# Performance work log

Measured on AMD Instinct MI355X. Metric: run time of the kernel, lower is better.

The kernel has to match this reference:

```python
import jax, jax.numpy as jnp
import numpy as np

N_NODES = 10000
N_EDGES = 160000
IN_DIM, HID_DIM, OUT_DIM = 256, 512, 256


def gcn_conv(x, W, b, src, dst, dinv):
    # PyG GCNConv with add_self_loops=True and symmetric normalization.
    # dinv = deg^{-1/2} computed once (degrees include self loops).
    h = x @ W                                   # [N, F_out]
    norm = dinv[src] * dinv[dst]                # [E]
    msg = h[src] * norm[:, None]                # gather + scale, [E, F_out]
    agg = jnp.zeros_like(h).at[dst].add(msg)    # scatter-add over edges
    agg = agg + h * (dinv * dinv)[:, None]      # self-loop contribution
    return agg + b


def setup_inputs() -> dict:
    key = jax.random.key(0)
    ks = jax.random.split(key, 8)
    x = jax.random.normal(ks[0], (N_NODES, IN_DIM), dtype=jnp.float32)
    edge_index = jax.random.randint(ks[1], (2, N_EDGES), 0, N_NODES, dtype=jnp.int64)

    def glorot(k, fan_in, fan_out):
        s = jnp.sqrt(6.0 / (fan_in + fan_out)).astype(jnp.float32)
        return jax.random.uniform(k, (fan_in, fan_out), jnp.float32, -s, s)

    return {
        "x": x,
        "W1": glorot(ks[2], IN_DIM, HID_DIM), "b1": jnp.zeros((HID_DIM,), jnp.float32),
        "W2": glorot(ks[3], HID_DIM, HID_DIM), "b2": jnp.zeros((HID_DIM,), jnp.float32),
        "W3": glorot(ks[4], HID_DIM, OUT_DIM), "b3": jnp.zeros((OUT_DIM,), jnp.float32),
        "edge_index": edge_index,
    }


def reference(x, W1, b1, W2, b2, W3, b3, edge_index):
    src, dst = edge_index[0], edge_index[1]
    n = x.shape[0]
    # degree with self loops (edge weight 1), shared by all three layers
    deg = jnp.zeros((n,), x.dtype).at[dst].add(1.0) + 1.0
    dinv = jax.lax.rsqrt(deg)
    h = jnp.tanh(gcn_conv(x, W1, b1, src, dst, dinv))
    h = jnp.tanh(gcn_conv(h, W2, b2, src, dst, dinv))
    out = gcn_conv(h, W3, b3, src, dst, dinv)
    return out
```

## Files before the change

kernel.cpp:

```cpp
#include <hip/hip_runtime.h>
#include <math.h>

#define NN 10000
#define NE 160000
#define IN_DIM 256
#define HID_DIM 512
#define OUT_DIM 256

typedef unsigned short u16;
typedef _Float16 f16x8 __attribute__((ext_vector_type(8)));
typedef __attribute__((ext_vector_type(4))) float f32x4;


union F16U { _Float16 h; u16 u; };
static __device__ __forceinline__ u16 f2h_bits(float f) {
    F16U v; v.h = (_Float16)f; return v.u;
}
static __device__ __forceinline__ float h2f(u16 b) {
    F16U v; v.u = b; return (float)v.h;
}


__global__ void k_init(const float* __restrict__ W1, const float* __restrict__ W2,
                       const float* __restrict__ W3,
                       u16* __restrict__ W1h, u16* __restrict__ W1l,
                       u16* __restrict__ W2h, u16* __restrict__ W2l,
                       u16* __restrict__ W3h, u16* __restrict__ W3l,
                       int* __restrict__ deg) {
    int idx = blockIdx.x * blockDim.x + threadIdx.x;
    const int S1 = IN_DIM * HID_DIM;
    const int S2 = HID_DIM * HID_DIM;
    const int S3 = HID_DIM * OUT_DIM;
    const int TW = S1 + S2 + S3;
    if (idx < TW) {
        const float* W; u16 *Th, *Tl; int K, N, local;
        if (idx < S1)           { W = W1; Th = W1h; Tl = W1l; K = IN_DIM;  N = HID_DIM; local = idx; }
        else if (idx < S1 + S2) { W = W2; Th = W2h; Tl = W2l; K = HID_DIM; N = HID_DIM; local = idx - S1; }
        else                    { W = W3; Th = W3h; Tl = W3l; K = HID_DIM; N = OUT_DIM; local = idx - S1 - S2; }
        int k = local / N, n = local - k * N;
        float v = W[local];
        F16U hh; hh.h = (_Float16)v;
        float r = (v - (float)hh.h) * 2048.0f;
        Th[(size_t)n * K + k] = hh.u;
        Tl[(size_t)n * K + k] = f2h_bits(r);
    } else if (idx < TW + NN) {
        deg[idx - TW] = 0;
    }
}


__global__ void k_count_deg(const int* __restrict__ dst, int* __restrict__ deg) {
    int e = blockIdx.x * blockDim.x + threadIdx.x;
    if (e < NE) atomicAdd(&deg[dst[e]], 1);
}

__launch_bounds__(1024)
__global__ void k_scan(const int* __restrict__ deg, int* __restrict__ row,
                       int* __restrict__ csr, float* __restrict__ dinv) {
    __shared__ int sdeg[10240];
    __shared__ int sums[1024];
    const int tid = threadIdx.x;
    for (int i = tid; i < NN; i += 1024) sdeg[i] = deg[i];
    __syncthreads();
    const int CH = 10;
    int base = tid * CH;
    int s = 0;
    for (int j = 0; j < CH; ++j) {
        int i = base + j;
        if (i < NN) s += sdeg[i] + 1;
    }
    sums[tid] = s;
    __syncthreads();
    for (int off = 1; off < 1024; off <<= 1) {
        int t = (tid >= off) ? sums[tid - off] : 0;
        __syncthreads();
        sums[tid] += t;
        __syncthreads();
    }
    int run = sums[tid] - s;
    for (int j = 0; j < CH; ++j) {
        int i = base + j;
        if (i < NN) {
            int dg = sdeg[i];
            csr[run] = i;
            row[i] = run + 1;
            dinv[i] = rsqrtf((float)dg + 1.0f);
            run += dg + 1;
        }
    }
}

__global__ void k_fill(const int* __restrict__ src, const int* __restrict__ dst,
                       int* __restrict__ row, int* __restrict__ csr) {
    int e = blockIdx.x * blockDim.x + threadIdx.x;
    if (e < NE) {
        int pos = atomicAdd(&row[dst[e]], 1);
        csr[pos] = src[e];
    }
}


struct PfSet { uint4 a0, a1, bh, bl; };

template<int K, bool HAS_BIAS, bool DO_TANH, bool F16_OUT, bool ROWSCALE>
__launch_bounds__(256)
__global__ void k_gemm_f16x2(const u16* __restrict__ A, const u16* __restrict__ Bhi,
                             const u16* __restrict__ Blo,
                             const float* __restrict__ bias, const float* __restrict__ rowscale,
                             float* __restrict__ C, u16* __restrict__ Ch,
                             int M, int N, int MT, int MT8) {
    __shared__ uint4 As[2][512];
    __shared__ uint4 BsH[2][256];
    __shared__ uint4 BsL[2][256];

    const int id = blockIdx.x;
    const int xcd = id & 7;
    const int q2 = id >> 3;
    const int mt = (q2 % MT8) * 8 + xcd;
    const int nt = q2 / MT8;
    if (mt >= MT) return;

    const int tid  = threadIdx.x;
    const int wave = tid >> 6;
    const int lane = tid & 63;
    const int lr   = lane & 15;
    const int quad = lane >> 4;
    const int m_base = mt * 128;
    const int n_base = nt * 64;

    const int s_row = tid >> 2;
    const int s_kq  = tid & 3;
    const int c_lo  = ((s_row >> 4) << 6) + s_kq * 16 + (s_row & 15);

    const u16* pA0 = A   + (size_t)(m_base + s_row) * K + s_kq * 8;
    const u16* pA1 = pA0 + (size_t)64 * K;
    const u16* pBh = Bhi + (size_t)(n_base + s_row) * K + s_kq * 8;
    const u16* pBl = Blo + (size_t)(n_base + s_row) * K + s_kq * 8;
    const bool g0 = (m_base + s_row) < M;
    const bool g1 = (m_base + s_row + 64) < M;

    const uint4 z = make_uint4(0u, 0u, 0u, 0u);

    auto load_set = [&](int it, PfSet& r) {
        const int ko = it * 32;
        r.a0 = z; r.a1 = z;
        if (g0) r.a0 = *(const uint4*)(pA0 + ko);
        if (g1) r.a1 = *(const uint4*)(pA1 + ko);
        r.bh = *(const uint4*)(pBh + ko);
        r.bl = *(const uint4*)(pBl + ko);
    };
    auto lds_write = [&](int buf, const PfSet& r) {
        As[buf][c_lo] = r.a0;
        As[buf][c_lo + 256] = r.a1;
        BsH[buf][c_lo] = r.bh;
        BsL[buf][c_lo] = r.bl;
    };

    f32x4 accH[2][4] = {};
    f32x4 accL[2][4] = {};

    auto compute = [&](int buf) {
        f16x8 a[2], bH[4], bL[4];
#pragma unroll
        for (int tm = 0; tm < 2; ++tm) {
            int c = (wave * 2 + tm) * 64 + lane;
            a[tm] = *(const f16x8*)&As[buf][c];
        }
#pragma unroll
        for (int tn = 0; tn < 4; ++tn) {
            int c = tn * 64 + lane;
            bH[tn] = *(const f16x8*)&BsH[buf][c];
            bL[tn] = *(const f16x8*)&BsL[buf][c];
        }
#pragma unroll
        for (int tm = 0; tm < 2; ++tm)
#pragma unroll
            for (int tn = 0; tn < 4; ++tn) {
                accH[tm][tn] = __builtin_amdgcn_mfma_f32_16x16x32_f16(a[tm], bH[tn], accH[tm][tn], 0, 0, 0);
                accL[tm][tn] = __builtin_amdgcn_mfma_f32_16x16x32_f16(a[tm], bL[tn], accL[tm][tn], 0, 0, 0);
            }
    };

    const int NIT = K >> 5;
    PfSet sA;

    load_set(0, sA);
    lds_write(0, sA);
    __syncthreads();

    for (int it = 0; it < NIT; ++it) {
        const bool has_next = (it + 1) < NIT;
        PfSet sN;
        if (has_next) load_set(it + 1, sN);
        compute(it & 1);
        if (has_next) lds_write((it + 1) & 1, sN);
        __syncthreads();
    }

#pragma unroll
    for (int tm = 0; tm < 2; ++tm) {
        int row0 = m_base + wave * 32 + tm * 16 + quad * 4;
#pragma unroll
        for (int i = 0; i < 4; ++i) {
            int row = row0 + i;
            if (row >= M) continue;
            float rs = ROWSCALE ? rowscale[row] : 1.0f;
#pragma unroll
            for (int tn = 0; tn < 4; ++tn) {
                int col = n_base + tn * 16 + lr;
                float v = accH[tm][tn][i] + accL[tm][tn][i] * (1.0f / 2048.0f);
                if (HAS_BIAS) v += bias[col];
                if (DO_TANH) v = tanhf(v);
                if (ROWSCALE) v *= rs;
                if (F16_OUT) {
                    Ch[(size_t)row * N + col] = f2h_bits(v);
                } else {
                    C[(size_t)row * N + col] = v;
                }
            }
        }
    }
}


template<bool PRESCALED, bool HAS_BIAS, bool F16_OUT, int F4>
__launch_bounds__(256)
__global__ void k_gather(const float* __restrict__ h, const float* __restrict__ dinv,
                         const int* __restrict__ row_end, const int* __restrict__ csr,
                         const float* __restrict__ bias,
                         float* __restrict__ outF, u16* __restrict__ outH) {
    constexpr int NS = 8;
    constexpr int F4S = F4 / NS;
    constexpr int NPB = 256 / F4S;
    const int slice = blockIdx.x & (NS - 1);
    const int g = blockIdx.x >> 3;
    const int tid = threadIdx.x;
    const int d = g * NPB + tid / F4S;
    if (d >= NN) return;
    const int f = slice * F4S + (tid & (F4S - 1));

    const int start = (d == 0) ? 0 : row_end[d - 1];
    const int end = row_end[d];
    const float4* h4 = (const float4*)h;

    float ax = 0.f, ay = 0.f, az = 0.f, aw = 0.f;
    int e = start;
    for (; e + 8 <= end; e += 8) {
        int s[8]; float4 v[8]; float w[8];
#pragma unroll
        for (int j = 0; j < 8; ++j) s[j] = csr[e + j];
#pragma unroll
        for (int j = 0; j < 8; ++j) v[j] = h4[(size_t)s[j] * F4 + f];
#pragma unroll
        for (int j = 0; j < 8; ++j) w[j] = PRESCALED ? 1.0f : dinv[s[j]];
#pragma unroll
        for (int j = 0; j < 8; ++j) {
            ax += w[j] * v[j].x; ay += w[j] * v[j].y;
            az += w[j] * v[j].z; aw += w[j] * v[j].w;
        }
    }
    for (; e < end; ++e) {
        int s = csr[e];
        float w = PRESCALED ? 1.0f : dinv[s];
        float4 v = h4[(size_t)s * F4 + f];
        ax += w * v.x; ay += w * v.y; az += w * v.z; aw += w * v.w;
    }

    const float dd = dinv[d];
    float rx = dd * ax, ry = dd * ay, rz = dd * az, rw = dd * aw;
    if (HAS_BIAS) {
        float4 bv = ((const float4*)bias)[f];
        rx += bv.x; ry += bv.y; rz += bv.z; rw += bv.w;
    }
    if (F16_OUT) {
        ushort4 vh = make_ushort4(f2h_bits(rx), f2h_bits(ry), f2h_bits(rz), f2h_bits(rw));
        ((ushort4*)outH)[(size_t)d * F4 + f] = vh;
    } else {
        ((float4*)outF)[(size_t)d * F4 + f] = make_float4(rx, ry, rz, rw);
    }
}


extern "C" void kernel_launch(void* const* d_in, const int* in_sizes, int n_in,
                              void* d_out, int out_size, void* d_ws, size_t ws_size,
                              hipStream_t stream) {
    const float* x  = (const float*)d_in[0];
    const float* W1 = (const float*)d_in[1];
    const float* b1 = (const float*)d_in[2];
    const float* W2 = (const float*)d_in[3];
    const float* b2 = (const float*)d_in[4];
    const float* W3 = (const float*)d_in[5];
    const float* b3 = (const float*)d_in[6];
    const int* edge = (const int*)d_in[7];
    const int* src = edge;
    const int* dst = edge + NE;
    float* out = (float*)d_out;

    const size_t SLOT = (size_t)NN * HID_DIM * 4;
    char* p = (char*)d_ws;
    char* slot0 = p;
    char* slot1 = p + SLOT;
    char* q = p + 2 * SLOT;
    u16* W1Th = (u16*)q; q += (size_t)IN_DIM  * HID_DIM * 2;
    u16* W1Tl = (u16*)q; q += (size_t)IN_DIM  * HID_DIM * 2;
    u16* W2Th = (u16*)q; q += (size_t)HID_DIM * HID_DIM * 2;
    u16* W2Tl = (u16*)q; q += (size_t)HID_DIM * HID_DIM * 2;
    u16* W3Th = (u16*)q; q += (size_t)HID_DIM * OUT_DIM * 2;
    u16* W3Tl = (u16*)q; q += (size_t)HID_DIM * OUT_DIM * 2;
    int*   deg  = (int*)q;   q += (size_t)NN * 4;
    float* dinv = (float*)q; q += (size_t)NN * 4;
    int*   row  = (int*)q;   q += (size_t)NN * 4;
    int*   csr  = (int*)q;   q += (size_t)(NE + NN) * 4;

    u16* Xagg   = (u16*)slot0;
    float* g1   = (float*)slot1;
    u16* H1agg  = (u16*)slot0;
    u16* h2     = (u16*)slot1;
    float* g3   = (float*)slot0;

    const int T = 256;
    const int MT = (NN + 127) / 128;
    const int MT8 = (MT + 7) / 8;

    {
        int total = IN_DIM * HID_DIM + HID_DIM * HID_DIM + HID_DIM * OUT_DIM + NN;
        k_init<<<(total + T - 1) / T, T, 0, stream>>>(W1, W2, W3, W1Th, W1Tl,
                                                      W2Th, W2Tl, W3Th, W3Tl, deg);
    }
    k_count_deg<<<(NE + T - 1) / T, T, 0, stream>>>(dst, deg);
    k_scan<<<1, 1024, 0, stream>>>(deg, row, csr, dinv);
    k_fill<<<(NE + T - 1) / T, T, 0, stream>>>(src, dst, row, csr);

    const int G256 = ((NN + 31) / 32) * 8;
    const int G512 = ((NN + 15) / 16) * 8;
    const int GEMM_G512 = 8 * MT8 * (HID_DIM / 64);
    const int GEMM_G256 = 8 * MT8 * (OUT_DIM / 64);

    k_gather<false, false, true, IN_DIM / 4><<<G256, 256, 0, stream>>>(
        x, dinv, row, csr, nullptr, nullptr, Xagg);
    k_gemm_f16x2<IN_DIM, true, true, false, true><<<GEMM_G512, 256, 0, stream>>>(
        Xagg, W1Th, W1Tl, b1, dinv, g1, nullptr, NN, HID_DIM, MT, MT8);

    k_gather<true, false, true, HID_DIM / 4><<<G512, 256, 0, stream>>>(
        g1, dinv, row, csr, nullptr, nullptr, H1agg);
    k_gemm_f16x2<HID_DIM, true, true, true, false><<<GEMM_G512, 256, 0, stream>>>(
        H1agg, W2Th, W2Tl, b2, nullptr, nullptr, h2, NN, HID_DIM, MT, MT8);

    k_gemm_f16x2<HID_DIM, false, false, false, true><<<GEMM_G256, 256, 0, stream>>>(
        h2, W3Th, W3Tl, nullptr, dinv, g3, nullptr, NN, OUT_DIM, MT, MT8);
    k_gather<true, true, false, OUT_DIM / 4><<<G256, 256, 0, stream>>>(
        g3, dinv, row, csr, b3, out, nullptr);

    (void)in_sizes; (void)n_in; (void)out_size; (void)ws_size;
}
```

Baseline: 236.2 us.

## Store gathered node features in fp16 to halve sparse aggregation traffic

All gather inputs now come from fp16 buffers: x is converted to fp16 in the init kernel, and the GEMMs that feed a gather write fp16 instead of fp32. The gather kernel reads 8 halves per 16-byte load, accumulates in fp32, and each block covers twice as many nodes. This cuts the bytes moved by the bandwidth-bound random gathers roughly in half. The cost is an extra pass converting x and fp16 rounding of intermediate features, which reduces accuracy.

```diff
diff --git a/kernel.cpp b/kernel.cpp
--- a/kernel.cpp
+++ b/kernel.cpp
@@ -16,22 +16,20 @@
 static __device__ __forceinline__ u16 f2h_bits(float f) {
     F16U v; v.h = (_Float16)f; return v.u;
 }
-static __device__ __forceinline__ float h2f(u16 b) {
-    F16U v; v.u = b; return (float)v.h;
-}
 
 
 __global__ void k_init(const float* __restrict__ W1, const float* __restrict__ W2,
-                       const float* __restrict__ W3,
+                       const float* __restrict__ W3, const float* __restrict__ x,
                        u16* __restrict__ W1h, u16* __restrict__ W1l,
                        u16* __restrict__ W2h, u16* __restrict__ W2l,
                        u16* __restrict__ W3h, u16* __restrict__ W3l,
-                       int* __restrict__ deg) {
+                       u16* __restrict__ xh, int* __restrict__ deg) {
     int idx = blockIdx.x * blockDim.x + threadIdx.x;
     const int S1 = IN_DIM * HID_DIM;
     const int S2 = HID_DIM * HID_DIM;
     const int S3 = HID_DIM * OUT_DIM;
     const int TW = S1 + S2 + S3;
+    const int TX = NN * IN_DIM;
     if (idx < TW) {
         const float* W; u16 *Th, *Tl; int K, N, local;
         if (idx < S1)           { W = W1; Th = W1h; Tl = W1l; K = IN_DIM;  N = HID_DIM; local = idx; }
@@ -43,8 +41,11 @@
         float r = (v - (float)hh.h) * 2048.0f;
         Th[(size_t)n * K + k] = hh.u;
         Tl[(size_t)n * K + k] = f2h_bits(r);
-    } else if (idx < TW + NN) {
-        deg[idx - TW] = 0;
+    } else if (idx < TW + TX) {
+        int j = idx - TW;
+        xh[j] = f2h_bits(x[j]);
+    } else if (idx < TW + TX + NN) {
+        deg[idx - TW - TX] = 0;
     }
 }
 
@@ -223,60 +224,69 @@
 }
 
 
-template<bool PRESCALED, bool HAS_BIAS, bool F16_OUT, int F4>
+template<bool PRESCALED, bool HAS_BIAS, bool F16_OUT, int F>
 __launch_bounds__(256)
-__global__ void k_gather(const float* __restrict__ h, const float* __restrict__ dinv,
-                         const int* __restrict__ row_end, const int* __restrict__ csr,
-                         const float* __restrict__ bias,
-                         float* __restrict__ outF, u16* __restrict__ outH) {
-    constexpr int NS = 8;
-    constexpr int F4S = F4 / NS;
-    constexpr int NPB = 256 / F4S;
-    const int slice = blockIdx.x & (NS - 1);
-    const int g = blockIdx.x >> 3;
+__global__ void k_gather_h(const u16* __restrict__ h, const float* __restrict__ dinv,
+                           const int* __restrict__ row_end, const int* __restrict__ csr,
+                           const float* __restrict__ bias,
+                           float* __restrict__ outF, u16* __restrict__ outH) {
+    constexpr int L  = F / 8;
+    constexpr int LS = L / 8;
+    constexpr int NPB = 256 / LS;
     const int tid = threadIdx.x;
-    const int d = g * NPB + tid / F4S;
+    const int d = (blockIdx.x >> 3) * NPB + tid / LS;
     if (d >= NN) return;
-    const int f = slice * F4S + (tid & (F4S - 1));
+    const int f8 = (blockIdx.x & 7) * LS + (tid & (LS - 1));
 
     const int start = (d == 0) ? 0 : row_end[d - 1];
     const int end = row_end[d];
-    const float4* h4 = (const float4*)h;
-
-    float ax = 0.f, ay = 0.f, az = 0.f, aw = 0.f;
+    const uint4* h16 = (const uint4*)h;
+
+    float acc[8] = {};
     int e = start;
     for (; e + 8 <= end; e += 8) {
-        int s[8]; float4 v[8]; float w[8];
+        int s[8]; uint4 raw[8]; float w[8];
 #pragma unroll
         for (int j = 0; j < 8; ++j) s[j] = csr[e + j];
 #pragma unroll
-        for (int j = 0; j < 8; ++j) v[j] = h4[(size_t)s[j] * F4 + f];
+        for (int j = 0; j < 8; ++j) raw[j] = h16[(size_t)s[j] * L + f8];
 #pragma unroll
         for (int j = 0; j < 8; ++j) w[j] = PRESCALED ? 1.0f : dinv[s[j]];
 #pragma unroll
         for (int j = 0; j < 8; ++j) {
-            ax += w[j] * v[j].x; ay += w[j] * v[j].y;
-            az += w[j] * v[j].z; aw += w[j] * v[j].w;
+            f16x8 hv = *(const f16x8*)&raw[j];
+#pragma unroll
+            for (int t = 0; t < 8; ++t) acc[t] += w[j] * (float)hv[t];
         }
     }
     for (; e < end; ++e) {
         int s = csr[e];
         float w = PRESCALED ? 1.0f : dinv[s];
-        float4 v = h4[(size_t)s * F4 + f];
-        ax += w * v.x; ay += w * v.y; az += w * v.z; aw += w * v.w;
+        uint4 raw = h16[(size_t)s * L + f8];
+        f16x8 hv = *(const f16x8*)&raw;
+#pragma unroll
+        for (int t = 0; t < 8; ++t) acc[t] += w * (float)hv[t];
     }
 
     const float dd = dinv[d];
-    float rx = dd * ax, ry = dd * ay, rz = dd * az, rw = dd * aw;
+    float r[8];
+#pragma unroll
+    for (int t = 0; t < 8; ++t) r[t] = dd * acc[t];
     if (HAS_BIAS) {
-        float4 bv = ((const float4*)bias)[f];
-        rx += bv.x; ry += bv.y; rz += bv.z; rw += bv.w;
+        const float4* b4 = (const float4*)bias;
+        float4 b0 = b4[f8 * 2], b1 = b4[f8 * 2 + 1];
+        r[0] += b0.x; r[1] += b0.y; r[2] += b0.z; r[3] += b0.w;
+        r[4] += b1.x; r[5] += b1.y; r[6] += b1.z; r[7] += b1.w;
     }
     if (F16_OUT) {
-        ushort4 vh = make_ushort4(f2h_bits(rx), f2h_bits(ry), f2h_bits(rz), f2h_bits(rw));
-        ((ushort4*)outH)[(size_t)d * F4 + f] = vh;
+        union { u16 a[8]; uint4 v; } pk;
+#pragma unroll
+        for (int t = 0; t < 8; ++t) pk.a[t] = f2h_bits(r[t]);
+        ((uint4*)outH)[(size_t)d * L + f8] = pk.v;
     } else {
-        ((float4*)outF)[(size_t)d * F4 + f] = make_float4(rx, ry, rz, rw);
+        size_t base = (size_t)d * (F / 4) + f8 * 2;
+        ((float4*)outF)[base]     = make_float4(r[0], r[1], r[2], r[3]);
+        ((float4*)outF)[base + 1] = make_float4(r[4], r[5], r[6], r[7]);
     }
 }
 
@@ -311,45 +321,47 @@
     float* dinv = (float*)q; q += (size_t)NN * 4;
     int*   row  = (int*)q;   q += (size_t)NN * 4;
     int*   csr  = (int*)q;   q += (size_t)(NE + NN) * 4;
-
-    u16* Xagg   = (u16*)slot0;
-    float* g1   = (float*)slot1;
-    u16* H1agg  = (u16*)slot0;
-    u16* h2     = (u16*)slot1;
-    float* g3   = (float*)slot0;
+    u16*   xh   = (u16*)q;   q += (size_t)NN * IN_DIM * 2;
+
+    u16* Xagg  = (u16*)slot0;
+    u16* g1h   = (u16*)slot1;
+    u16* H1agg = (u16*)slot0;
+    u16* h2    = (u16*)slot1;
+    u16* g3h   = (u16*)slot0;
 
     const int T = 256;
     const int MT = (NN + 127) / 128;
     const int MT8 = (MT + 7) / 8;
 
     {
-        int total = IN_DIM * HID_DIM + HID_DIM * HID_DIM + HID_DIM * OUT_DIM + NN;
-        k_init<<<(total + T - 1) / T, T, 0, stream>>>(W1, W2, W3, W1Th, W1Tl,
-                                                      W2Th, W2Tl, W3Th, W3Tl, deg);
+        int total = IN_DIM * HID_DIM + HID_DIM * HID_DIM + HID_DIM * OUT_DIM
+                  + NN * IN_DIM + NN;
+        k_init<<<(total + T - 1) / T, T, 0, stream>>>(W1, W2, W3, x, W1Th, W1Tl,
+                                                      W2Th, W2Tl, W3Th, W3Tl, xh, deg);
     }
     k_count_deg<<<(NE + T - 1) / T, T, 0, stream>>>(dst, deg);
     k_scan<<<1, 1024, 0, stream>>>(deg, row, csr, dinv);
     k_fill<<<(NE + T - 1) / T, T, 0, stream>>>(src, dst, row, csr);
 
-    const int G256 = ((NN + 31) / 32) * 8;
-    const int G512 = ((NN + 15) / 16) * 8;
+    const int G256 = ((NN + 63) / 64) * 8;
+    const int G512 = ((NN + 31) / 32) * 8;
     const int GEMM_G512 = 8 * MT8 * (HID_DIM / 64);
     const int GEMM_G256 = 8 * MT8 * (OUT_DIM / 64);
 
-    k_gather<false, false, true, IN_DIM / 4><<<G256, 256, 0, stream>>>(
-        x, dinv, row, csr, nullptr, nullptr, Xagg);
-    k_gemm_f16x2<IN_DIM, true, true, false, true><<<GEMM_G512, 256, 0, stream>>>(
-        Xagg, W1Th, W1Tl, b1, dinv, g1, nullptr, NN, HID_DIM, MT, MT8);
-
-    k_gather<true, false, true, HID_DIM / 4><<<G512, 256, 0, stream>>>(
-        g1, dinv, row, csr, nullptr, nullptr, H1agg);
+    k_gather_h<false, false, true, IN_DIM><<<G256, 256, 0, stream>>>(
+        xh, dinv, row, csr, nullptr, nullptr, Xagg);
+    k_gemm_f16x2<IN_DIM, true, true, true, true><<<GEMM_G512, 256, 0, stream>>>(
+        Xagg, W1Th, W1Tl, b1, dinv, nullptr, g1h, NN, HID_DIM, MT, MT8);
+
+    k_gather_h<true, false, true, HID_DIM><<<G512, 256, 0, stream>>>(
+        g1h, dinv, row, csr, nullptr, nullptr, H1agg);
     k_gemm_f16x2<HID_DIM, true, true, true, false><<<GEMM_G512, 256, 0, stream>>>(
         H1agg, W2Th, W2Tl, b2, nullptr, nullptr, h2, NN, HID_DIM, MT, MT8);
 
-    k_gemm_f16x2<HID_DIM, false, false, false, true><<<GEMM_G256, 256, 0, stream>>>(
-        h2, W3Th, W3Tl, nullptr, dinv, g3, nullptr, NN, OUT_DIM, MT, MT8);
-    k_gather<true, true, false, OUT_DIM / 4><<<G256, 256, 0, stream>>>(
-        g3, dinv, row, csr, b3, out, nullptr);
+    k_gemm_f16x2<HID_DIM, false, false, true, true><<<GEMM_G256, 256, 0, stream>>>(
+        h2, W3Th, W3Tl, nullptr, dinv, nullptr, g3h, NN, OUT_DIM, MT, MT8);
+    k_gather_h<true, true, false, OUT_DIM><<<G256, 256, 0, stream>>>(
+        g3h, dinv, row, csr, b3, out, nullptr);
 
     (void)in_sizes; (void)n_in; (void)out_size; (void)ws_size;
 }
```

New measurement: 226.2 us (median of 2 runs). -4.3%, faster.
